# Performance work log

Measured on AMD Instinct MI355X. Metric: run time of the kernel, lower is better.

Reference implementation:

```python
import jax, jax.numpy as jnp
import numpy as np
from jax import lax

NUM_CLUSTER = 128
N_ITERS = 10


def setup_inputs() -> dict:
    key = jax.random.key(0)
    feat_g = jax.random.normal(key, (131072, 256), dtype=jnp.float32)
    return {"feat_g": feat_g}


def _sq_dists(x, c):
    x2 = jnp.sum(x * x, axis=1, keepdims=True)            # [N,1]
    c2 = jnp.sum(c * c, axis=1)                           # [K]
    return x2 - 2.0 * (x @ c.T) + c2[None, :]


def _kmeans_fit(x, k, iters):
    n = x.shape[0]
    init_c = x[:k]  # deterministic init: first k points
    ones = jnp.ones((n,), dtype=x.dtype)

    def step(c, _):
        assign = jnp.argmin(_sq_dists(x, c), axis=1)                 # [N]
        sums = jax.ops.segment_sum(x, assign, num_segments=k)       # [K,d]
        counts = jax.ops.segment_sum(ones, assign, num_segments=k)  # [K]
        new_c = sums / jnp.maximum(counts, 1.0)[:, None]
        new_c = jnp.where(counts[:, None] > 0, new_c, c)  # keep empty clusters
        return new_c, None

    c, _ = lax.scan(step, init_c, None, length=iters)
    return c


def reference(feat_g):
    # view(batch, -1, dim) then view(-1, dim) is an identity reshape for the math
    x = lax.stop_gradient(feat_g)  # original detaches feat_gc before fit/predict
    c = _kmeans_fit(x, NUM_CLUSTER, N_ITERS)
    preds = jnp.argmin(_sq_dists(x, c), axis=1)  # [N] int labels
    return preds
```

## Files before the change

kernel.cpp:

```cpp
#include <hip/hip_runtime.h>

#define NPTS 131072
#define DIM 256
#define NK 128
#define NITER 10
#define SEG 16
#define SLICES 64
#define PTS_PER_SLICE (NPTS / SLICES)
#define CHUNK 128

typedef _Float16 half8 __attribute__((ext_vector_type(8)));
typedef _Float16 half4v __attribute__((ext_vector_type(4)));
typedef float f32x4 __attribute__((ext_vector_type(4)));

#define RSCALE 4096.0f
#define RINV 2.44140625e-4f

__global__ void x2_kernel(const float* __restrict__ x, float* __restrict__ x2) {
  int tid = threadIdx.x;
  int p = blockIdx.x * 16 + (tid >> 4);
  int part = tid & 15;
  const float4* xr = (const float4*)(x + (size_t)p * DIM);
  float s = 0.f;
#pragma unroll
  for (int j = 0; j < 4; ++j) {
    float4 v = xr[part * 4 + j];
    s += v.x * v.x;
    s += v.y * v.y;
    s += v.z * v.z;
    s += v.w * v.w;
  }
#pragma unroll
  for (int m = 8; m >= 1; m >>= 1) s += __shfl_xor(s, m, 16);
  if (part == 0) x2[p] = s;
}

__global__ void c2_kernel(const float* __restrict__ c, float* __restrict__ c2) {
  int k = blockIdx.x, lane = threadIdx.x;
  float4 v = ((const float4*)(c + (size_t)k * DIM))[lane];
  float s = v.x * v.x + v.y * v.y + v.z * v.z + v.w * v.w;
#pragma unroll
  for (int m = 32; m >= 1; m >>= 1) s += __shfl_xor(s, m, 64);
  if (lane == 0) c2[k] = s;
}

__global__ void convert_x2_kernel(const float* __restrict__ x, _Float16* __restrict__ x1,
                                  _Float16* __restrict__ x2s, float* __restrict__ x2) {
  int tid = threadIdx.x;
  int p = blockIdx.x * 16 + (tid >> 4);
  int part = tid & 15;
  const float4* xr = (const float4*)(x + (size_t)p * DIM);
  half8* o1 = (half8*)(x1 + (size_t)p * DIM);
  half8* o2 = (half8*)(x2s + (size_t)p * DIM);
  float s = 0.f;
  half8 hh[2], ll[2];
#pragma unroll
  for (int j = 0; j < 4; ++j) {
    float4 v = xr[part * 4 + j];
    float f[4] = {v.x, v.y, v.z, v.w};
#pragma unroll
    for (int u = 0; u < 4; ++u) {
      _Float16 hi = (_Float16)f[u];
      float r = f[u] - (float)hi;
      hh[j >> 1][(j & 1) * 4 + u] = hi;
      ll[j >> 1][(j & 1) * 4 + u] = (_Float16)(r * RSCALE);
      s += f[u] * f[u];
    }
  }
#pragma unroll
  for (int jj = 0; jj < 2; ++jj) {
    o1[part * 2 + jj] = hh[jj];
    o2[part * 2 + jj] = ll[jj];
  }
#pragma unroll
  for (int m = 8; m >= 1; m >>= 1) s += __shfl_xor(s, m, 16);
  if (part == 0) x2[p] = s;
}

__global__ void convert_c_kernel(const float* __restrict__ c, _Float16* __restrict__ ct) {
  int i = blockIdx.x * 256 + threadIdx.x;
  int k = i >> 6;
  int d4 = i & 63;
  float4 v = ((const float4*)c)[i];
  float f[4] = {v.x, v.y, v.z, v.w};
  half4v h, l;
#pragma unroll
  for (int j = 0; j < 4; ++j) {
    _Float16 hi = (_Float16)f[j];
    float r = f[j] - (float)hi;
    h[j] = hi;
    l[j] = (_Float16)(r * RSCALE);
  }
  int ch = d4 >> 3;
  int idx4 = ch * 2048 + k * 8 + (d4 & 7);
  ((half4v*)ct)[idx4] = h;
  ((half4v*)ct)[idx4 + 1024] = l;
}

template <bool DOHIST>
__global__ __launch_bounds__(256, 2) void assign_mfma_kernel(
    const _Float16* __restrict__ x1, const _Float16* __restrict__ x2s,
    const _Float16* __restrict__ ct, const float* __restrict__ x2,
    const float* __restrict__ c2, int* __restrict__ out, int* __restrict__ counts) {
  __shared__ __align__(16) _Float16 cbuf[2][8192];
  __shared__ int hcnt[NK];

  int tid = threadIdx.x;
  int lane = tid & 63;
  int w = tid >> 6;
  int lcol = lane & 15;
  int lgrp = lane >> 4;
  int row0 = blockIdx.x * 128 + w * 32;

  if (DOHIST && tid < NK) hcnt[tid] = 0;

  const _Float16* xa = x1 + (size_t)(row0 + lcol) * DIM + lgrp * 8;
  const _Float16* xb = x2s + (size_t)(row0 + lcol) * DIM + lgrp * 8;
  const half8* ctv = (const half8*)ct;

  f32x4 acc1[2][8], acc2[2][8];
#pragma unroll
  for (int rt = 0; rt < 2; ++rt)
#pragma unroll
    for (int c8 = 0; c8 < 8; ++c8) {
      acc1[rt][c8] = f32x4{0.f, 0.f, 0.f, 0.f};
      acc2[rt][c8] = f32x4{0.f, 0.f, 0.f, 0.f};
    }

  half8 A1[2], A2[2], nA1[2], nA2[2], sreg[4];

#pragma unroll
  for (int r = 0; r < 4; ++r) sreg[r] = ctv[r * 256 + tid];
#pragma unroll
  for (int rt = 0; rt < 2; ++rt) {
    A1[rt] = *(const half8*)(xa + rt * 16 * DIM);
    A2[rt] = *(const half8*)(xb + rt * 16 * DIM);
  }
#pragma unroll
  for (int r = 0; r < 4; ++r) ((half8*)cbuf[0])[r * 256 + tid] = sreg[r];
  __syncthreads();

#pragma unroll
  for (int ck = 0; ck < 8; ++ck) {
    const int cb = ck & 1;
    if (ck < 7) {
#pragma unroll
      for (int r = 0; r < 4; ++r) sreg[r] = ctv[(ck + 1) * 1024 + r * 256 + tid];
#pragma unroll
      for (int rt = 0; rt < 2; ++rt) {
        nA1[rt] = *(const half8*)(xa + rt * 16 * DIM + (ck + 1) * 32);
        nA2[rt] = *(const half8*)(xb + rt * 16 * DIM + (ck + 1) * 32);
      }
    }
#pragma unroll
    for (int c8 = 0; c8 < 8; ++c8) {
      int bidx = (c8 * 16 + lcol) * 32 + lgrp * 8;
      half8 b1 = *(const half8*)&cbuf[cb][bidx];
      half8 b2 = *(const half8*)&cbuf[cb][4096 + bidx];
#pragma unroll
      for (int rt = 0; rt < 2; ++rt) {
        acc1[rt][c8] = __builtin_amdgcn_mfma_f32_16x16x32_f16(A1[rt], b1, acc1[rt][c8], 0, 0, 0);
        acc2[rt][c8] = __builtin_amdgcn_mfma_f32_16x16x32_f16(A1[rt], b2, acc2[rt][c8], 0, 0, 0);
        acc2[rt][c8] = __builtin_amdgcn_mfma_f32_16x16x32_f16(A2[rt], b1, acc2[rt][c8], 0, 0, 0);
      }
    }
    if (ck < 7) {
#pragma unroll
      for (int r = 0; r < 4; ++r) ((half8*)cbuf[cb ^ 1])[r * 256 + tid] = sreg[r];
#pragma unroll
      for (int rt = 0; rt < 2; ++rt) {
        A1[rt] = nA1[rt];
        A2[rt] = nA2[rt];
      }
      __syncthreads();
    }
  }

#pragma unroll
  for (int rt = 0; rt < 2; ++rt) {
    int pbase = row0 + rt * 16 + lgrp * 4;
    float x2p[4];
#pragma unroll
    for (int r = 0; r < 4; ++r) x2p[r] = x2[pbase + r];
    float bv[4];
    int bk[4];
#pragma unroll
    for (int r = 0; r < 4; ++r) { bv[r] = 3.4e38f; bk[r] = 0; }
#pragma unroll
    for (int c8 = 0; c8 < 8; ++c8) {
      int kc = c8 * 16 + lcol;
      float c2k = c2[kc];
#pragma unroll
      for (int r = 0; r < 4; ++r) {
        float dot = fmaf(acc2[rt][c8][r], RINV, acc1[rt][c8][r]);
        float d = fmaf(-2.f, dot, x2p[r]) + c2k;
        if (d < bv[r]) { bv[r] = d; bk[r] = kc; }
      }
    }
#pragma unroll
    for (int m = 1; m <= 8; m <<= 1) {
#pragma unroll
      for (int r = 0; r < 4; ++r) {
        float ov = __shfl_xor(bv[r], m, 64);
        int ok = __shfl_xor(bk[r], m, 64);
        if (ov < bv[r] || (ov == bv[r] && ok < bk[r])) { bv[r] = ov; bk[r] = ok; }
      }
    }
    if (lcol == 0) {
#pragma unroll
      for (int r = 0; r < 4; ++r) {
        out[pbase + r] = bk[r];
        if (DOHIST) atomicAdd(&hcnt[bk[r]], 1);
      }
    }
  }

  if (DOHIST) {
    __syncthreads();
    if (tid < NK) {
      int v = hcnt[tid];
      if (v) atomicAdd(&counts[tid], v);
    }
  }
}

__global__ __launch_bounds__(256, 2) void csum_kernel(
    const _Float16* __restrict__ x1, const _Float16* __restrict__ x2s,
    const int* __restrict__ assignb, float* __restrict__ p) {
  __shared__ __align__(16) _Float16 bt[2][2][32][136];
  __shared__ int abuf[2][CHUNK];

  int tid = threadIdx.x;
  int lane = tid & 63;
  int w = tid >> 6;
  int slice = blockIdx.x;
  int d0 = blockIdx.y * 32;
  int ibase = slice * PTS_PER_SLICE;
  int kbase = w * 32;
  int lcol = lane & 15;
  int lgrp = lane >> 4;

  int sarr = tid >> 7;
  int srow = tid & 127;
  const _Float16* xsrc = sarr ? x2s : x1;

  f32x4 acc1[2][2], acc2[2][2];
#pragma unroll
  for (int kt = 0; kt < 2; ++kt)
#pragma unroll
    for (int dt = 0; dt < 2; ++dt) {
      acc1[kt][dt] = f32x4{0.f, 0.f, 0.f, 0.f};
      acc2[kt][dt] = f32x4{0.f, 0.f, 0.f, 0.f};
    }

  {
    const half8* src = (const half8*)(xsrc + (size_t)(ibase + srow) * DIM + d0);
    half8 v[4];
#pragma unroll
    for (int q = 0; q < 4; ++q) v[q] = src[q];
#pragma unroll
    for (int q = 0; q < 4; ++q)
#pragma unroll
      for (int j = 0; j < 8; ++j) bt[0][sarr][q * 8 + j][srow] = v[q][j];
    if (tid < 32) ((int4*)abuf[0])[tid] = ((const int4*)(assignb + ibase))[tid];
  }
  __syncthreads();

  const int NCH = PTS_PER_SLICE / CHUNK;
  for (int ci = 0; ci < NCH; ++ci) {
    const int cb = ci & 1;
    half8 nv[4];
    int4 na;
    bool more = (ci < NCH - 1);
    if (more) {
      const half8* src =
          (const half8*)(xsrc + (size_t)(ibase + (ci + 1) * CHUNK + srow) * DIM + d0);
#pragma unroll
      for (int q = 0; q < 4; ++q) nv[q] = src[q];
      if (tid < 32) na = ((const int4*)(assignb + ibase + (ci + 1) * CHUNK))[tid];
    }

#pragma unroll
    for (int ks = 0; ks < 4; ++ks) {
      int4 av0 = ((int4*)abuf[cb])[ks * 8 + lgrp * 2];
      int4 av1 = ((int4*)abuf[cb])[ks * 8 + lgrp * 2 + 1];
      int aj[8] = {av0.x, av0.y, av0.z, av0.w, av1.x, av1.y, av1.z, av1.w};
      half8 oh[2];
#pragma unroll
      for (int kt = 0; kt < 2; ++kt) {
        int kk = kbase + kt * 16 + lcol;
#pragma unroll
        for (int j = 0; j < 8; ++j) oh[kt][j] = (aj[j] == kk) ? (_Float16)1.0f : (_Float16)0.0f;
      }
#pragma unroll
      for (int dt = 0; dt < 2; ++dt) {
        half8 b1 = *(const half8*)&bt[cb][0][dt * 16 + lcol][ks * 32 + lgrp * 8];
        half8 b2 = *(const half8*)&bt[cb][1][dt * 16 + lcol][ks * 32 + lgrp * 8];
#pragma unroll
        for (int kt = 0; kt < 2; ++kt) {
          acc1[kt][dt] = __builtin_amdgcn_mfma_f32_16x16x32_f16(oh[kt], b1, acc1[kt][dt], 0, 0, 0);
          acc2[kt][dt] = __builtin_amdgcn_mfma_f32_16x16x32_f16(oh[kt], b2, acc2[kt][dt], 0, 0, 0);
        }
      }
    }

    if (more) {
      __syncthreads();
#pragma unroll
      for (int q = 0; q < 4; ++q)
#pragma unroll
        for (int j = 0; j < 8; ++j) bt[cb ^ 1][sarr][q * 8 + j][srow] = nv[q][j];
      if (tid < 32) ((int4*)abuf[cb ^ 1])[tid] = na;
      __syncthreads();
    }
  }

#pragma unroll
  for (int kt = 0; kt < 2; ++kt)
#pragma unroll
    for (int dt = 0; dt < 2; ++dt) {
      int dd = d0 + dt * 16 + lcol;
#pragma unroll
      for (int r = 0; r < 4; ++r) {
        int krow = kbase + kt * 16 + lgrp * 4 + r;
        p[((size_t)slice * NK + krow) * DIM + dd] =
            fmaf(acc2[kt][dt][r], RINV, acc1[kt][dt][r]);
      }
    }
}

__global__ void reduce_v4_kernel(const float* __restrict__ p, int* __restrict__ counts,
                                 float* __restrict__ c, float* __restrict__ c2,
                                 _Float16* __restrict__ ct) {
  __shared__ float wsum[4];
  int k = blockIdx.x, d = threadIdx.x;
  int cnt = counts[k];
  float s = 0.f;
#pragma unroll 4
  for (int sl = 0; sl < SLICES; ++sl) s += p[((size_t)sl * NK + k) * DIM + d];

  float nc;
  if (cnt > 0)
    nc = s / fmaxf((float)cnt, 1.0f);
  else
    nc = c[(size_t)k * DIM + d];
  c[(size_t)k * DIM + d] = nc;

  {
    _Float16 hi = (_Float16)nc;
    float r = nc - (float)hi;
    _Float16 lov = (_Float16)(r * RSCALE);
    int ch = d >> 5, dd = d & 31;
    ct[ch * 8192 + k * 32 + dd] = hi;
    ct[ch * 8192 + k * 32 + dd + 4096] = lov;
  }

  float sq = nc * nc;
#pragma unroll
  for (int m = 32; m >= 1; m >>= 1) sq += __shfl_xor(sq, m, 64);
  if ((threadIdx.x & 63) == 0) wsum[threadIdx.x >> 6] = sq;
  __syncthreads();
  if (threadIdx.x == 0) {
    c2[k] = wsum[0] + wsum[1] + wsum[2] + wsum[3];
    counts[k] = 0;
  }
}

__global__ void assign_kernel(const float* __restrict__ x, const float* __restrict__ c,
                              const float* __restrict__ x2, const float* __restrict__ c2,
                              int* __restrict__ assign_out) {
  __shared__ float4 xs4[64 * 4];
  __shared__ float4 cs4[128 * 4];
  __shared__ float redv[64][17];
  __shared__ int redk[64][17];

  int tid = threadIdx.x;
  int tx = tid & 15;
  int ty = tid >> 4;
  int row0 = blockIdx.x * 64;

  float acc[4][8];
#pragma unroll
  for (int a = 0; a < 4; ++a)
#pragma unroll
    for (int b = 0; b < 8; ++b) acc[a][b] = 0.f;

  for (int ck = 0; ck < 16; ++ck) {
    {
      int p = tid >> 2, d4 = tid & 3;
      float4 v = *(const float4*)(x + (size_t)(row0 + p) * DIM + ck * 16 + d4 * 4);
      xs4[p * 4 + (d4 ^ ((p >> 2) & 3))] = v;
    }
#pragma unroll
    for (int r = 0; r < 2; ++r) {
      int idx = tid + r * 256;
      int kk = idx >> 2, dd = idx & 3;
      float4 v = *(const float4*)(c + (size_t)kk * DIM + ck * 16 + dd * 4);
      cs4[kk * 4 + (dd ^ ((kk >> 3) & 3))] = v;
    }
    __syncthreads();
#pragma unroll
    for (int d4 = 0; d4 < 4; ++d4) {
      float4 xr[4], cr[8];
#pragma unroll
      for (int pp = 0; pp < 4; ++pp) xr[pp] = xs4[(tx * 4 + pp) * 4 + (d4 ^ (tx & 3))];
#pragma unroll
      for (int kk = 0; kk < 8; ++kk) cr[kk] = cs4[(ty * 8 + kk) * 4 + (d4 ^ (ty & 3))];
#pragma unroll
      for (int pp = 0; pp < 4; ++pp)
#pragma unroll
        for (int kk = 0; kk < 8; ++kk) {
          acc[pp][kk] = fmaf(xr[pp].x, cr[kk].x, acc[pp][kk]);
          acc[pp][kk] = fmaf(xr[pp].y, cr[kk].y, acc[pp][kk]);
          acc[pp][kk] = fmaf(xr[pp].z, cr[kk].z, acc[pp][kk]);
          acc[pp][kk] = fmaf(xr[pp].w, cr[kk].w, acc[pp][kk]);
        }
    }
    __syncthreads();
  }

  float x2p[4];
#pragma unroll
  for (int pp = 0; pp < 4; ++pp) x2p[pp] = x2[row0 + tx * 4 + pp];

  float bestv[4];
  int bestk[4];
#pragma unroll
  for (int pp = 0; pp < 4; ++pp) { bestv[pp] = 3.4e38f; bestk[pp] = 0; }
#pragma unroll
  for (int kk = 0; kk < 8; ++kk) {
    float c2k = c2[ty * 8 + kk];
#pragma unroll
    for (int pp = 0; pp < 4; ++pp) {
      float d = fmaf(-2.f, acc[pp][kk], x2p[pp]) + c2k;
      if (d < bestv[pp]) { bestv[pp] = d; bestk[pp] = ty * 8 + kk; }
    }
  }
#pragma unroll
  for (int pp = 0; pp < 4; ++pp) {
    redv[tx * 4 + pp][ty] = bestv[pp];
    redk[tx * 4 + pp][ty] = bestk[pp];
  }
  __syncthreads();
  if (tid < 64) {
    float bv = redv[tid][0];
    int bk = redk[tid][0];
#pragma unroll
    for (int t = 1; t < 16; ++t) {
      float v = redv[tid][t];
      if (v < bv) { bv = v; bk = redk[tid][t]; }
    }
    assign_out[row0 + tid] = bk;
  }
}

__global__ void hist_kernel(const int* __restrict__ assign_in, int* __restrict__ hist) {
  __shared__ int h[NK];
  int tid = threadIdx.x, b = blockIdx.x;
  if (tid < NK) h[tid] = 0;
  __syncthreads();
#pragma unroll
  for (int r = 0; r < 4; ++r) {
    int a = assign_in[b * 1024 + r * 256 + tid];
    atomicAdd(&h[a], 1);
  }
  __syncthreads();
  if (tid < NK) hist[b * NK + tid] = h[tid];
}

__global__ void scan_fb_kernel(const int* __restrict__ hist, int* __restrict__ base,
                               int* __restrict__ counts, int* __restrict__ cbase) {
  __shared__ int h[128 * NK];
  int tid = threadIdx.x;
  for (int i = tid; i < 128 * NK; i += 256) h[i] = hist[i];
  __syncthreads();
  if (tid < NK) {
    int run = 0;
    for (int b = 0; b < 128; ++b) {
      int v = h[b * NK + tid];
      h[b * NK + tid] = run;
      run += v;
    }
    counts[tid] = run;
  }
  __syncthreads();
  if (tid == 0) {
    int cb = 0;
    for (int j = 0; j < NK; ++j) {
      cbase[j] = cb;
      cb += counts[j];
    }
  }
  __syncthreads();
  if (tid < NK) {
    int cbk = cbase[tid];
    for (int b = 0; b < 128; ++b) base[b * NK + tid] = h[b * NK + tid] + cbk;
  }
}

__global__ void scatter_kernel(const int* __restrict__ assign_in, const int* __restrict__ base,
                               int* __restrict__ perm) {
  __shared__ int cnt[NK];
  int lane = threadIdx.x, b = blockIdx.x;
  cnt[lane] = base[b * NK + lane];
  cnt[lane + 64] = base[b * NK + lane + 64];
  for (int r = 0; r < 16; ++r) {
    int p = b * 1024 + r * 64 + lane;
    int a = assign_in[p];
    unsigned long long mask = ~0ull;
#pragma unroll
    for (int j = 0; j < 7; ++j) {
      unsigned long long bal = __ballot((a >> j) & 1);
      mask &= ((a >> j) & 1) ? bal : ~bal;
    }
    int rank = __popcll(mask & ((1ull << lane) - 1ull));
    int pos = cnt[a] + rank;
    perm[pos] = p;
    if (rank == 0) cnt[a] += (int)__popcll(mask);
  }
}

__global__ void seg_sum_kernel(const float* __restrict__ x, const int* __restrict__ perm,
                               const int* __restrict__ counts, const int* __restrict__ cbase,
                               float* __restrict__ partial) {
  int k = blockIdx.x, s = blockIdx.y, d = threadIdx.x;
  int cnt = counts[k], off = cbase[k];
  int j0 = (int)(((long long)cnt * s) / SEG);
  int j1 = (int)(((long long)cnt * (s + 1)) / SEG);
  float sum = 0.f;
  int j = j0;
  for (; j + 4 <= j1; j += 4) {
    int p0 = perm[off + j + 0];
    int p1 = perm[off + j + 1];
    int p2 = perm[off + j + 2];
    int p3 = perm[off + j + 3];
    sum += x[(size_t)p0 * DIM + d];
    sum += x[(size_t)p1 * DIM + d];
    sum += x[(size_t)p2 * DIM + d];
    sum += x[(size_t)p3 * DIM + d];
  }
  for (; j < j1; ++j) sum += x[(size_t)perm[off + j] * DIM + d];
  partial[((size_t)k * SEG + s) * DIM + d] = sum;
}

__global__ void reduce_fb_kernel(const float* __restrict__ partial, const int* __restrict__ counts,
                                 float* __restrict__ c, float* __restrict__ c2) {
  __shared__ float wsum[4];
  int k = blockIdx.x, d = threadIdx.x;
  int cnt = counts[k];
  float s = 0.f;
#pragma unroll
  for (int t = 0; t < SEG; ++t) s += partial[((size_t)k * SEG + t) * DIM + d];
  float nc;
  if (cnt > 0)
    nc = s / fmaxf((float)cnt, 1.0f);
  else
    nc = c[(size_t)k * DIM + d];
  c[(size_t)k * DIM + d] = nc;
  float s2 = nc * nc;
#pragma unroll
  for (int m = 32; m >= 1; m >>= 1) s2 += __shfl_xor(s2, m, 64);
  if ((threadIdx.x & 63) == 0) wsum[threadIdx.x >> 6] = s2;
  __syncthreads();
  if (threadIdx.x == 0) c2[k] = wsum[0] + wsum[1] + wsum[2] + wsum[3];
}

extern "C" void kernel_launch(void* const* d_in, const int* in_sizes, int n_in,
                              void* d_out, int out_size, void* d_ws, size_t ws_size,
                              hipStream_t stream) {
  const float* x = (const float*)d_in[0];
  char* ws = (char*)d_ws;

  const size_t NEED_BIG = 143918080;
  bool use_mfma = ws_size >= NEED_BIG;

  if (use_mfma) {
    _Float16* x1 = (_Float16*)(ws + 0);
    _Float16* x2s = (_Float16*)(ws + 67108864);
    float* c = (float*)(ws + 134217728);
    _Float16* ct = (_Float16*)(ws + 134348800);
    float* c2 = (float*)(ws + 134479872);
    float* x2 = (float*)(ws + 134480384);
    int* assignb = (int*)(ws + 135004672);
    int* counts = (int*)(ws + 135528960);
    float* p = (float*)(ws + 135529472);

    hipMemcpyAsync(c, x, (size_t)NK * DIM * sizeof(float), hipMemcpyDeviceToDevice, stream);
    hipMemsetAsync(counts, 0, NK * sizeof(int), stream);
    convert_x2_kernel<<<NPTS / 16, 256, 0, stream>>>(x, x1, x2s, x2);
    c2_kernel<<<NK, 64, 0, stream>>>(c, c2);
    convert_c_kernel<<<NK * DIM / 4 / 256, 256, 0, stream>>>(c, ct);

    for (int it = 0; it < NITER; ++it) {
      assign_mfma_kernel<true>
          <<<NPTS / 128, 256, 0, stream>>>(x1, x2s, ct, x2, c2, assignb, counts);
      csum_kernel<<<dim3(SLICES, DIM / 32), 256, 0, stream>>>(x1, x2s, assignb, p);
      reduce_v4_kernel<<<NK, 256, 0, stream>>>(p, counts, c, c2, ct);
    }
    assign_mfma_kernel<false>
        <<<NPTS / 128, 256, 0, stream>>>(x1, x2s, ct, x2, c2, (int*)d_out, counts);
  } else {
    float* c = (float*)(ws + 0);
    float* c2 = (float*)(ws + 131072);
    float* x2 = (float*)(ws + 132096);
    int* assignb = (int*)(ws + 656384);
    int* hist = (int*)(ws + 1180672);
    int* base = (int*)(ws + 1246208);
    int* counts = (int*)(ws + 1311744);
    int* cbase = (int*)(ws + 1312256);
    int* perm = (int*)(ws + 1312768);
    float* partial = (float*)(ws + 1837056);

    hipMemcpyAsync(c, x, (size_t)NK * DIM * sizeof(float), hipMemcpyDeviceToDevice, stream);
    x2_kernel<<<NPTS / 16, 256, 0, stream>>>(x, x2);
    c2_kernel<<<NK, 64, 0, stream>>>(c, c2);

    for (int it = 0; it < NITER; ++it) {
      assign_kernel<<<NPTS / 64, 256, 0, stream>>>(x, c, x2, c2, assignb);
      hist_kernel<<<NPTS / 1024, 256, 0, stream>>>(assignb, hist);
      scan_fb_kernel<<<1, 256, 0, stream>>>(hist, base, counts, cbase);
      scatter_kernel<<<NPTS / 1024, 64, 0, stream>>>(assignb, base, perm);
      seg_sum_kernel<<<dim3(NK, SEG), 256, 0, stream>>>(x, perm, counts, cbase, partial);
      reduce_fb_kernel<<<NK, 256, 0, stream>>>(partial, counts, c, c2);
    }
    assign_kernel<<<NPTS / 64, 256, 0, stream>>>(x, c, x2, c2, (int*)d_out);
  }
}
```

Measured before the change: 1.002 ms.

## Cut assign kernel registers: fold correction accumulator, async LDS loads, higher occupancy

```diff
diff --git a/kernel.cpp b/kernel.cpp
--- a/kernel.cpp
+++ b/kernel.cpp
@@ -98,7 +98,7 @@
 }
 
 template <bool DOHIST>
-__global__ __launch_bounds__(256, 2) void assign_mfma_kernel(
+__global__ __launch_bounds__(256, 4) void assign_mfma_kernel(
     const _Float16* __restrict__ x1, const _Float16* __restrict__ x2s,
     const _Float16* __restrict__ ct, const float* __restrict__ x2,
     const float* __restrict__ c2, int* __restrict__ out, int* __restrict__ counts) {
@@ -118,26 +118,18 @@
   const _Float16* xb = x2s + (size_t)(row0 + lcol) * DIM + lgrp * 8;
   const half8* ctv = (const half8*)ct;
 
-  f32x4 acc1[2][8], acc2[2][8];
+  f32x4 acc1[2][8];
 #pragma unroll
   for (int rt = 0; rt < 2; ++rt)
 #pragma unroll
-    for (int c8 = 0; c8 < 8; ++c8) {
-      acc1[rt][c8] = f32x4{0.f, 0.f, 0.f, 0.f};
-      acc2[rt][c8] = f32x4{0.f, 0.f, 0.f, 0.f};
-    }
-
-  half8 A1[2], A2[2], nA1[2], nA2[2], sreg[4];
-
-#pragma unroll
-  for (int r = 0; r < 4; ++r) sreg[r] = ctv[r * 256 + tid];
-#pragma unroll
-  for (int rt = 0; rt < 2; ++rt) {
-    A1[rt] = *(const half8*)(xa + rt * 16 * DIM);
-    A2[rt] = *(const half8*)(xb + rt * 16 * DIM);
-  }
-#pragma unroll
-  for (int r = 0; r < 4; ++r) ((half8*)cbuf[0])[r * 256 + tid] = sreg[r];
+    for (int c8 = 0; c8 < 8; ++c8) acc1[rt][c8] = f32x4{0.f, 0.f, 0.f, 0.f};
+
+#pragma unroll
+  for (int r = 0; r < 4; ++r) {
+    __builtin_amdgcn_global_load_lds(
+        (const __attribute__((address_space(1))) void*)(ctv + r * 256 + tid),
+        (__attribute__((address_space(3))) void*)&((half8*)cbuf[0])[r * 256 + tid], 16, 0, 0);
+  }
   __syncthreads();
 
 #pragma unroll
@@ -145,12 +137,18 @@
     const int cb = ck & 1;
     if (ck < 7) {
 #pragma unroll
-      for (int r = 0; r < 4; ++r) sreg[r] = ctv[(ck + 1) * 1024 + r * 256 + tid];
-#pragma unroll
-      for (int rt = 0; rt < 2; ++rt) {
-        nA1[rt] = *(const half8*)(xa + rt * 16 * DIM + (ck + 1) * 32);
-        nA2[rt] = *(const half8*)(xb + rt * 16 * DIM + (ck + 1) * 32);
-      }
+      for (int r = 0; r < 4; ++r) {
+        __builtin_amdgcn_global_load_lds(
+            (const __attribute__((address_space(1))) void*)(ctv + (ck + 1) * 1024 + r * 256 + tid),
+            (__attribute__((address_space(3))) void*)&((half8*)cbuf[cb ^ 1])[r * 256 + tid], 16, 0,
+            0);
+      }
+    }
+    half8 A1[2], A2[2];
+#pragma unroll
+    for (int rt = 0; rt < 2; ++rt) {
+      A1[rt] = *(const half8*)(xa + rt * 16 * DIM + ck * 32);
+      A2[rt] = *(const half8*)(xb + rt * 16 * DIM + ck * 32);
     }
 #pragma unroll
     for (int c8 = 0; c8 < 8; ++c8) {
@@ -160,20 +158,14 @@
 #pragma unroll
       for (int rt = 0; rt < 2; ++rt) {
         acc1[rt][c8] = __builtin_amdgcn_mfma_f32_16x16x32_f16(A1[rt], b1, acc1[rt][c8], 0, 0, 0);
-        acc2[rt][c8] = __builtin_amdgcn_mfma_f32_16x16x32_f16(A1[rt], b2, acc2[rt][c8], 0, 0, 0);
-        acc2[rt][c8] = __builtin_amdgcn_mfma_f32_16x16x32_f16(A2[rt], b1, acc2[rt][c8], 0, 0, 0);
-      }
-    }
-    if (ck < 7) {
-#pragma unroll
-      for (int r = 0; r < 4; ++r) ((half8*)cbuf[cb ^ 1])[r * 256 + tid] = sreg[r];
-#pragma unroll
-      for (int rt = 0; rt < 2; ++rt) {
-        A1[rt] = nA1[rt];
-        A2[rt] = nA2[rt];
-      }
-      __syncthreads();
-    }
+        f32x4 t = {0.f, 0.f, 0.f, 0.f};
+        t = __builtin_amdgcn_mfma_f32_16x16x32_f16(A1[rt], b2, t, 0, 0, 0);
+        t = __builtin_amdgcn_mfma_f32_16x16x32_f16(A2[rt], b1, t, 0, 0, 0);
+#pragma unroll
+        for (int r = 0; r < 4; ++r) acc1[rt][c8][r] = fmaf(t[r], RINV, acc1[rt][c8][r]);
+      }
+    }
+    __syncthreads();
   }
 
 #pragma unroll
@@ -192,8 +184,7 @@
       float c2k = c2[kc];
 #pragma unroll
       for (int r = 0; r < 4; ++r) {
-        float dot = fmaf(acc2[rt][c8][r], RINV, acc1[rt][c8][r]);
-        float d = fmaf(-2.f, dot, x2p[r]) + c2k;
+        float d = fmaf(-2.f, acc1[rt][c8][r], x2p[r]) + c2k;
         if (d < bv[r]) { bv[r] = d; bk[r] = kc; }
       }
     }
@@ -224,7 +215,7 @@
   }
 }
 
-__global__ __launch_bounds__(256, 2) void csum_kernel(
+__global__ __launch_bounds__(256, 4) void csum_kernel(
     const _Float16* __restrict__ x1, const _Float16* __restrict__ x2s,
     const int* __restrict__ assignb, float* __restrict__ p) {
   __shared__ __align__(16) _Float16 bt[2][2][32][136];
@@ -323,8 +314,7 @@
 #pragma unroll
       for (int r = 0; r < 4; ++r) {
         int krow = kbase + kt * 16 + lgrp * 4 + r;
-        p[((size_t)slice * NK + krow) * DIM + dd] =
-            fmaf(acc2[kt][dt][r], RINV, acc1[kt][dt][r]);
+        p[((size_t)slice * NK + krow) * DIM + dd] = fmaf(acc2[kt][dt][r], RINV, acc1[kt][dt][r]);
       }
     }
 }
```

After: 1.123 ms. 12.1% more time.
